# Optimization experiments

Hardware: AMD Instinct MI355X
Metric: run time of the kernel (lower is better)

The kernel has to match this reference:

```python
import jax, jax.numpy as jnp
import numpy as np

N, D_IN, D_HID, D_OUT, E = 8192, 1024, 4096, 1024, 8
N_ACTIVE = max(1, int(E * 0.625))  # 5
TEMP = float(np.e)               # temperature = np.e in source


def setup_inputs() -> dict:
    key = jax.random.key(0)
    ks = jax.random.split(key, 4)
    return {
        "x": jax.random.normal(ks[0], (N, D_IN), jnp.float32),
        "gate_w": jax.random.normal(ks[1], (D_IN, E), jnp.float32) * 0.02,
        "gate_b": jnp.zeros((E,), jnp.float32),
        "w1": jax.random.normal(ks[2], (E, D_IN, D_HID), jnp.float32) * 0.02,
        "b1": jnp.zeros((E, D_HID), jnp.float32),
        "w2": jax.random.normal(ks[3], (E, D_HID, D_OUT), jnp.float32) * 0.02,
        "b2": jnp.zeros((E, D_OUT), jnp.float32),
    }


def reference(x, gate_w, gate_b, w1, b1, w2, b2):
    # Gate: softmax over experts at temperature e, then top-k mask + renormalize
    scores = (x @ gate_w + gate_b) / TEMP                 # [N, E]
    probs = jax.nn.softmax(scores, axis=-1)               # [N, E]
    _, topk_idx = jax.lax.top_k(probs, N_ACTIVE)          # [N, k]
    mask = jax.nn.one_hot(topk_idx, E, dtype=probs.dtype).sum(axis=-2)  # [N, E]
    weights = probs * mask
    weights = weights / (weights.sum(axis=-1, keepdims=True) + 1e-8)
    # Dense all-experts FFN (dropout is eval-mode identity)
    h = jax.nn.relu(jnp.einsum('nd,edh->neh', x, w1) + b1)   # [N, E, d_hid]
    e_out = jnp.einsum('neh,eho->neo', h, w2) + b2           # [N, E, d_out]
    # Camp A (first E/2 experts) added, camp G subtracted: out = out_a - out_g
    sign = jnp.where(jnp.arange(E) < E // 2, 1.0, -1.0)      # [E]
    return jnp.einsum('ne,neo->no', weights * sign, e_out)   # [N, d_out]
```

## Files before the change

kernel.cpp:

```cpp
#include <hip/hip_runtime.h>
#include <hip/hip_bf16.h>
#include <cmath>


typedef _Float16 f16;
typedef _Float16 f16x8 __attribute__((ext_vector_type(8)));
typedef _Float16 f16x4 __attribute__((ext_vector_type(4)));
typedef float f32x4 __attribute__((ext_vector_type(4)));

#define NROWS 8192
#define DIN   1024
#define DHID  4096
#define DOUT  1024
#define NEXP  8

#define OFF_SGATE 0u
#define OFF_XH    262144u
#define OFF_W1T   17039360u
#define OFF_W2T   84148224u
#define OFF_P1    151257088u
#define OFF_HH    184811520u
#define NEED_NE2  319029248ull

__device__ __forceinline__ void gload_lds16(const void* gsrc, void* ldsdst) {
  __builtin_amdgcn_global_load_lds(
      (const __attribute__((address_space(1))) unsigned int*)gsrc,
      (__attribute__((address_space(3))) unsigned int*)ldsdst, 16, 0, 0);
}

__global__ void gate_kernel(const float* __restrict__ x,
                            const float* __restrict__ gw,
                            const float* __restrict__ gb,
                            float* __restrict__ sgate) {
  const int row = blockIdx.x * 4 + (threadIdx.x >> 6);
  const int l = threadIdx.x & 63;
  const float* xr = x + (size_t)row * DIN;
  float acc[8] = {0.f,0.f,0.f,0.f,0.f,0.f,0.f,0.f};
#pragma unroll
  for (int j = 0; j < 16; ++j) {
    const int k = l + 64 * j;
    const float xv = xr[k];
    const float4 g0 = *(const float4*)(gw + (size_t)k * 8);
    const float4 g1 = *(const float4*)(gw + (size_t)k * 8 + 4);
    acc[0] += xv * g0.x; acc[1] += xv * g0.y; acc[2] += xv * g0.z; acc[3] += xv * g0.w;
    acc[4] += xv * g1.x; acc[5] += xv * g1.y; acc[6] += xv * g1.z; acc[7] += xv * g1.w;
  }
#pragma unroll
  for (int off = 32; off > 0; off >>= 1) {
#pragma unroll
    for (int e = 0; e < 8; ++e) acc[e] += __shfl_xor(acc[e], off, 64);
  }
  if (l == 0) {
    const float invT = 0.36787944117144233f;
    float p[8]; float mx = -1e30f;
#pragma unroll
    for (int e = 0; e < 8; ++e) { p[e] = (acc[e] + gb[e]) * invT; mx = fmaxf(mx, p[e]); }
    float S = 0.f;
#pragma unroll
    for (int e = 0; e < 8; ++e) { p[e] = expf(p[e] - mx); S += p[e]; }
    const float inv = 1.0f / S;
#pragma unroll
    for (int e = 0; e < 8; ++e) p[e] *= inv;
    bool keep[8] = {true,true,true,true,true,true,true,true};
    for (int t = 0; t < 3; ++t) {
      float pmin = 1e30f; int mi = -1;
      for (int e = 0; e < 8; ++e)
        if (keep[e] && (p[e] < pmin || (p[e] == pmin && e > mi))) { pmin = p[e]; mi = e; }
      keep[mi] = false;
    }
    float wsum = 0.f;
#pragma unroll
    for (int e = 0; e < 8; ++e) if (keep[e]) wsum += p[e];
    const float rinv = 1.0f / (wsum + 1e-8f);
#pragma unroll
    for (int e = 0; e < 8; ++e) {
      const float wv = keep[e] ? p[e] * rinv : 0.0f;
      sgate[(size_t)row * 8 + e] = (e < 4) ? wv : -wv;
    }
  }
}

__global__ void cvt_x_kernel(const float* __restrict__ x, f16* __restrict__ xh) {
  const size_t i = ((size_t)blockIdx.x * blockDim.x + threadIdx.x) * 4;
  const float4 v = *(const float4*)(x + i);
  f16x4 o = { (f16)v.x, (f16)v.y, (f16)v.z, (f16)v.w };
  *(f16x4*)(xh + i) = o;
}

__global__ void transpose_cvt(const float* __restrict__ in, f16* __restrict__ out,
                              int R, int C) {
  __shared__ float tile[32][33];
  const int e = blockIdx.z;
  const float* ine = in + (size_t)e * R * C;
  f16* oute = out + (size_t)e * R * C;
  const int c0 = blockIdx.x * 32, r0 = blockIdx.y * 32;
  const int tx = threadIdx.x, ty = threadIdx.y;
#pragma unroll
  for (int i = 0; i < 4; ++i)
    tile[ty + i * 8][tx] = ine[(size_t)(r0 + ty + i * 8) * C + c0 + tx];
  __syncthreads();
#pragma unroll
  for (int i = 0; i < 4; ++i)
    oute[(size_t)(c0 + ty + i * 8) * R + r0 + tx] = (f16)tile[tx][ty + i * 8];
}

#define MFMAOP(a_, b_, c_) __builtin_amdgcn_mfma_f32_16x16x32_f16(a_, b_, c_, 0, 0, 0)

template <int EPI>
__global__ __launch_bounds__(512, 2) void gemm8p(
    const f16* __restrict__ A, int lda,
    const f16* __restrict__ B, int ldb, int nt,
    long long khA, long long khB,
    const float* __restrict__ bias,
    f16* __restrict__ outH, int ldc,
    float* outP0, float* outP1, int p1w,
    const float* __restrict__ sgate, int expert, int gx) {
  __shared__ alignas(16) f16 lA[4 * 8192];
  __shared__ alignas(16) f16 lB[4 * 8192];
  const int tid = threadIdx.x;
  const int l = tid & 63, w = tid >> 6;
  const int wr = w >> 2, wc = w & 3;

  const int nwg = gridDim.x, cpx = nwg >> 3;
  const int lg = ((int)blockIdx.x & 7) * cpx + ((int)blockIdx.x >> 3);

  int m0, n0;
  const f16* Aeff = A;
  const f16* Beff = B;
  float* P = nullptr;
  bool pw = false;
  if constexpr (EPI == 1) {
    m0 = (lg / gx) * 256; n0 = (lg % gx) * 256;
  } else {
    const int xx = lg >> 5, cc = lg & 31;
    const int kh = xx >> 2;
    n0 = (cc & 3) * 256;
    m0 = (((xx & 3) << 3) + (cc >> 2)) * 256;
    Aeff = A + (size_t)kh * (size_t)khA;
    Beff = B + (size_t)kh * (size_t)khB;
    P = kh ? outP1 : outP0;
    pw = (p1w != 0);
  }

  const int srow = tid >> 3;
  const int sxc = (tid & 7) ^ (srow & 7);
  const f16* pA = Aeff + (size_t)(m0 + srow) * lda + sxc * 8;
  const f16* pB = Beff + (size_t)(n0 + srow) * ldb + sxc * 8;
  f16* const dA = lA + w * 512;
  f16* const dB = lB + w * 512;

#define STG_A(slot, h, tk) do { \
    const f16* s_ = pA + (size_t)(h) * 128 * lda + (size_t)(tk) * 64; \
    gload_lds16(s_,            dA + (slot) * 8192); \
    gload_lds16(s_ + 64 * lda, dA + (slot) * 8192 + 4096); \
  } while (0)
#define STG_B(slot, h, tk) do { \
    const f16* s_ = pB + (size_t)(h) * 128 * ldb + (size_t)(tk) * 64; \
    gload_lds16(s_,            dB + (slot) * 8192); \
    gload_lds16(s_ + 64 * ldb, dB + (slot) * 8192 + 4096); \
  } while (0)

  const int cg = l >> 4, xr = l & 7;
  const int ok0 = ((cg ^ xr) << 4);
  const int ok1 = (((4 + cg) ^ xr) << 4);
  const char* const baA = (const char*)lA + (l & 15) * 128;
  const char* const baB = (const char*)lB + (wc & 1) * 8192 + (l & 15) * 128;

#define RDA(CA, f, o) (*(const f16x8*)(baA + ((CA) + wr) * 16384 + (f) * 2048 + (o)))
#define RDB(CB, g, o) (*(const f16x8*)(baB + ((CB) + (wc >> 1)) * 16384 + (g) * 2048 + (o)))
#define SYNC() do { __builtin_amdgcn_s_barrier(); \
    asm volatile("s_waitcnt lgkmcnt(0)" ::: "memory"); \
    __builtin_amdgcn_sched_barrier(0); } while (0)
#define ENDPH() do { __builtin_amdgcn_s_setprio(0); \
    __builtin_amdgcn_s_barrier(); } while (0)
#define VM6() do { asm volatile("s_waitcnt vmcnt(6)" ::: "memory"); \
    __builtin_amdgcn_sched_barrier(0); } while (0)
#define VM0() do { asm volatile("s_waitcnt vmcnt(0)" ::: "memory"); \
    __builtin_amdgcn_sched_barrier(0); } while (0)
#define MM(f, g, ar, br) acc[f][g] = MFMAOP(ar, br, acc[f][g])

  f32x4 acc[8][4] = {};
  f16x8 aA0,aA1,aB0,aB1,aC0,aC1,aD0,aD1;
  f16x8 b00,b01,b10,b11,b20,b21,b30,b31;

#define TILEBODY(T, CA, CB, SB1, SB0n, SA0n, SA1n) do { \
     \
    aA0 = RDA(CA, 0, ok0); aA1 = RDA(CA, 0, ok1); \
    aB0 = RDA(CA, 1, ok0); aB1 = RDA(CA, 1, ok1); \
    aC0 = RDA(CA, 2, ok0); aC1 = RDA(CA, 2, ok1); \
    aD0 = RDA(CA, 3, ok0); aD1 = RDA(CA, 3, ok1); \
    b00 = RDB(CB, 0, ok0); b01 = RDB(CB, 0, ok1); \
    b10 = RDB(CB, 1, ok0); b11 = RDB(CB, 1, ok1); \
    if ((T) + 1 < nt) STG_B(SB1, 1, (T) + 1); \
    SYNC(); \
    __builtin_amdgcn_s_setprio(1); \
    MM(0,0,aA0,b00); MM(0,1,aA0,b10); MM(1,0,aB0,b00); MM(1,1,aB0,b10); \
    MM(2,0,aC0,b00); MM(2,1,aC0,b10); MM(3,0,aD0,b00); MM(3,1,aD0,b10); \
    MM(0,0,aA1,b01); MM(0,1,aA1,b11); MM(1,0,aB1,b01); MM(1,1,aB1,b11); \
    MM(2,0,aC1,b01); MM(2,1,aC1,b11); MM(3,0,aD1,b01); MM(3,1,aD1,b11); \
    ENDPH(); \
     \
    b20 = RDB(CB, 2, ok0); b21 = RDB(CB, 2, ok1); \
    b30 = RDB(CB, 3, ok0); b31 = RDB(CB, 3, ok1); \
    SYNC(); \
    __builtin_amdgcn_s_setprio(1); \
    MM(0,2,aA0,b20); MM(0,3,aA0,b30); MM(1,2,aB0,b20); MM(1,3,aB0,b30); \
    MM(2,2,aC0,b20); MM(2,3,aC0,b30); MM(3,2,aD0,b20); MM(3,3,aD0,b30); \
    MM(0,2,aA1,b21); MM(0,3,aA1,b31); MM(1,2,aB1,b21); MM(1,3,aB1,b31); \
    MM(2,2,aC1,b21); MM(2,3,aC1,b31); MM(3,2,aD1,b21); MM(3,3,aD1,b31); \
    ENDPH(); \
     \
    aA0 = RDA(CA, 4, ok0); aA1 = RDA(CA, 4, ok1); \
    aB0 = RDA(CA, 5, ok0); aB1 = RDA(CA, 5, ok1); \
    aC0 = RDA(CA, 6, ok0); aC1 = RDA(CA, 6, ok1); \
    aD0 = RDA(CA, 7, ok0); aD1 = RDA(CA, 7, ok1); \
    if ((T) + 2 < nt) STG_B(SB0n, 0, (T) + 2); \
    SYNC(); \
    __builtin_amdgcn_s_setprio(1); \
    MM(4,0,aA0,b00); MM(4,1,aA0,b10); MM(5,0,aB0,b00); MM(5,1,aB0,b10); \
    MM(6,0,aC0,b00); MM(6,1,aC0,b10); MM(7,0,aD0,b00); MM(7,1,aD0,b10); \
    MM(4,0,aA1,b01); MM(4,1,aA1,b11); MM(5,0,aB1,b01); MM(5,1,aB1,b11); \
    MM(6,0,aC1,b01); MM(6,1,aC1,b11); MM(7,0,aD1,b01); MM(7,1,aD1,b11); \
    ENDPH(); \
     \
    if ((T) + 2 < nt) { STG_A(SA0n, 0, (T) + 2); STG_A(SA1n, 1, (T) + 2); \
                        VM6(); } \
    else { VM0(); } \
    SYNC(); \
    __builtin_amdgcn_s_setprio(1); \
    MM(4,2,aA0,b20); MM(4,3,aA0,b30); MM(5,2,aB0,b20); MM(5,3,aB0,b30); \
    MM(6,2,aC0,b20); MM(6,3,aC0,b30); MM(7,2,aD0,b20); MM(7,3,aD0,b30); \
    MM(4,2,aA1,b21); MM(4,3,aA1,b31); MM(5,2,aB1,b21); MM(5,3,aB1,b31); \
    MM(6,2,aC1,b21); MM(6,3,aC1,b31); MM(7,2,aD1,b21); MM(7,3,aD1,b31); \
    ENDPH(); \
  } while (0)

  STG_A(0, 0, 0); STG_B(0, 0, 0); STG_A(1, 1, 0); STG_B(1, 1, 0);
  STG_A(2, 0, 1); STG_B(2, 0, 1); STG_A(3, 1, 1);
  asm volatile("s_waitcnt vmcnt(6)" ::: "memory");
  __builtin_amdgcn_s_barrier();

  for (int t = 0; t < nt; t += 2) {
    TILEBODY(t,     0, 0, 3, 0, 0, 1);
    TILEBODY(t + 1, 2, 2, 1, 2, 2, 3);
  }
  asm volatile("s_waitcnt vmcnt(0)" ::: "memory");

  if constexpr (EPI == 1) {
#pragma unroll
    for (int mi = 0; mi < 8; ++mi)
#pragma unroll
      for (int r = 0; r < 4; ++r) {
        const int row = m0 + wr * 128 + mi * 16 + (l >> 4) * 4 + r;
        const float sg = sgate[(size_t)row * 8 + expert];
#pragma unroll
        for (int ni = 0; ni < 4; ++ni) {
          const int col = n0 + wc * 64 + ni * 16 + (l & 15);
          const float v = acc[mi][ni][r] + bias[col];
          outH[(size_t)row * ldc + col] = (f16)(fmaxf(v, 0.0f) * sg);
        }
      }
  } else {
    float* const scr = (w < 4) ? (float*)lA + w * 4096
                               : (float*)lB + (w - 4) * 4096;
    const int hl = l >> 4, ll = l & 15;
#pragma unroll
    for (int p = 0; p < 2; ++p) {
#pragma unroll
      for (int mi4 = 0; mi4 < 4; ++mi4)
#pragma unroll
        for (int r = 0; r < 4; ++r) {
          const int rowl = mi4 * 16 + hl * 4 + r;
#pragma unroll
          for (int ni = 0; ni < 4; ++ni)
            scr[rowl * 64 + ni * 16 + ll] = acc[p * 4 + mi4][ni][r];
        }
#pragma unroll
      for (int i = 0; i < 16; ++i) {
        const int rowl = hl + i * 4;
        f32x4 v = *(const f32x4*)(scr + rowl * 64 + ll * 4);
        const int row = m0 + wr * 128 + p * 64 + rowl;
        const int col = n0 + wc * 64 + ll * 4;
        f32x4* gp = (f32x4*)(P + (size_t)row * 1024 + col);
        if (!pw) {
          const f32x4 g = *gp;
          v[0] += g[0]; v[1] += g[1]; v[2] += g[2]; v[3] += g[3];
        }
        *gp = v;
      }
    }
  }
#undef STG_A
#undef STG_B
#undef RDA
#undef RDB
#undef SYNC
#undef ENDPH
#undef VM6
#undef VM0
#undef MM
#undef TILEBODY
}

template <bool WITHP>
__global__ void finalize_out(const float* p0,
                             const float* __restrict__ p1,
                             const float* __restrict__ sgate,
                             const float* __restrict__ b2,
                             float* out) {
  const int i = blockIdx.x * 256 + threadIdx.x;
  const int n = i >> 8, c4 = i & 255;
  float4 a = make_float4(0.f, 0.f, 0.f, 0.f);
  if constexpr (WITHP) {
    const float4 u = ((const float4*)p0)[i];
    const float4 v = ((const float4*)p1)[i];
    a.x = u.x + v.x; a.y = u.y + v.y; a.z = u.z + v.z; a.w = u.w + v.w;
  }
  const float* sg = sgate + (size_t)n * 8;
#pragma unroll
  for (int e = 0; e < 8; ++e) {
    const float s = sg[e];
    const float4 bv = ((const float4*)(b2 + (size_t)e * 1024))[c4];
    a.x += s * bv.x; a.y += s * bv.y; a.z += s * bv.z; a.w += s * bv.w;
  }
  ((float4*)out)[i] = a;
}

extern "C" void kernel_launch(void* const* d_in, const int* in_sizes, int n_in,
                              void* d_out, int out_size, void* d_ws, size_t ws_size,
                              hipStream_t stream) {
  const float* x  = (const float*)d_in[0];
  const float* gw = (const float*)d_in[1];
  const float* gb = (const float*)d_in[2];
  const float* w1 = (const float*)d_in[3];
  const float* b1 = (const float*)d_in[4];
  const float* w2 = (const float*)d_in[5];
  const float* b2 = (const float*)d_in[6];
  float* out = (float*)d_out;

  char* ws = (char*)d_ws;
  float* sgate = (float*)(ws + OFF_SGATE);
  f16* xh  = (f16*)(ws + OFF_XH);
  f16* w1t = (f16*)(ws + OFF_W1T);
  f16* w2t = (f16*)(ws + OFF_W2T);
  float* p1 = (float*)(ws + OFF_P1);
  f16* hh  = (f16*)(ws + OFF_HH);

  const int NE = (ws_size >= NEED_NE2) ? 2 : 1;
  const int ngrp = NEXP / NE;

  gate_kernel<<<NROWS / 4, 256, 0, stream>>>(x, gw, gb, sgate);
  cvt_x_kernel<<<(NROWS * DIN) / (256 * 4), 256, 0, stream>>>(x, xh);
  transpose_cvt<<<dim3(DHID / 32, DIN / 32, NEXP), dim3(32, 8), 0, stream>>>(w1, w1t, DIN, DHID);
  transpose_cvt<<<dim3(DOUT / 32, DHID / 32, NEXP), dim3(32, 8), 0, stream>>>(w2, w2t, DHID, DOUT);

  const long long khA = (long long)NE * 2048;
  const long long khB = (NE == 2) ? (long long)DOUT * DHID
                                  : 2048LL;
  const int nt2 = NE * 32;
  for (int g = 0; g < ngrp; ++g) {
    for (int ei = 0; ei < NE; ++ei) {
      const int e = g * NE + ei;
      gemm8p<1><<<512, 512, 0, stream>>>(
          xh, DIN, w1t + (size_t)e * DHID * DIN, DIN, DIN / 64,
          0, 0,
          b1 + (size_t)e * DHID, hh + (size_t)ei * DHID, NE * DHID,
          nullptr, nullptr, 0, sgate, e, DHID / 256);
    }
    gemm8p<2><<<256, 512, 0, stream>>>(
        hh, NE * DHID, w2t + (size_t)g * NE * DOUT * DHID, DHID, nt2,
        khA, khB,
        nullptr, nullptr, 0, out, p1, (g == 0) ? 1 : 0, nullptr, 0, 0);
  }
  finalize_out<true><<<(NROWS * DOUT) / (256 * 4), 256, 0, stream>>>(
      out, p1, sgate, b2, out);
}
```

Measured before the change: 1.358 ms.

## Replace second-stage 256x256 GEMM with 128x128 tile kernel using more workgroups

The down-projection GEMM, which accumulates into the fp32 partial outputs, moves from the shared 256x256-tile, 512-thread kernel to a dedicated 128x128-tile, 256-thread kernel with double-buffered K=32 steps and 1024 workgroups. The first-stage kernel is specialised to its original epilogue. The aim is better occupancy and CU load balance for the second GEMM, which previously launched only 256 workgroups. In exchange, per-tile data reuse is lower, global traffic is higher, and the simpler pipeline waits on vmcnt(0) every K step.

```diff
diff --git a/kernel.cpp b/kernel.cpp
--- a/kernel.cpp
+++ b/kernel.cpp
@@ -106,14 +106,11 @@
 
 #define MFMAOP(a_, b_, c_) __builtin_amdgcn_mfma_f32_16x16x32_f16(a_, b_, c_, 0, 0, 0)
 
-template <int EPI>
-__global__ __launch_bounds__(512, 2) void gemm8p(
+__global__ __launch_bounds__(512, 2) void gemm8p1(
     const f16* __restrict__ A, int lda,
     const f16* __restrict__ B, int ldb, int nt,
-    long long khA, long long khB,
     const float* __restrict__ bias,
     f16* __restrict__ outH, int ldc,
-    float* outP0, float* outP1, int p1w,
     const float* __restrict__ sgate, int expert, int gx) {
   __shared__ alignas(16) f16 lA[4 * 8192];
   __shared__ alignas(16) f16 lB[4 * 8192];
@@ -123,29 +120,12 @@
 
   const int nwg = gridDim.x, cpx = nwg >> 3;
   const int lg = ((int)blockIdx.x & 7) * cpx + ((int)blockIdx.x >> 3);
-
-  int m0, n0;
-  const f16* Aeff = A;
-  const f16* Beff = B;
-  float* P = nullptr;
-  bool pw = false;
-  if constexpr (EPI == 1) {
-    m0 = (lg / gx) * 256; n0 = (lg % gx) * 256;
-  } else {
-    const int xx = lg >> 5, cc = lg & 31;
-    const int kh = xx >> 2;
-    n0 = (cc & 3) * 256;
-    m0 = (((xx & 3) << 3) + (cc >> 2)) * 256;
-    Aeff = A + (size_t)kh * (size_t)khA;
-    Beff = B + (size_t)kh * (size_t)khB;
-    P = kh ? outP1 : outP0;
-    pw = (p1w != 0);
-  }
+  const int m0 = (lg / gx) * 256, n0 = (lg % gx) * 256;
 
   const int srow = tid >> 3;
   const int sxc = (tid & 7) ^ (srow & 7);
-  const f16* pA = Aeff + (size_t)(m0 + srow) * lda + sxc * 8;
-  const f16* pB = Beff + (size_t)(n0 + srow) * ldb + sxc * 8;
+  const f16* pA = A + (size_t)(m0 + srow) * lda + sxc * 8;
+  const f16* pB = B + (size_t)(n0 + srow) * ldb + sxc * 8;
   f16* const dA = lA + w * 512;
   f16* const dB = lB + w * 512;
 
@@ -184,7 +164,6 @@
   f16x8 b00,b01,b10,b11,b20,b21,b30,b31;
 
 #define TILEBODY(T, CA, CB, SB1, SB0n, SA0n, SA1n) do { \
-     \
     aA0 = RDA(CA, 0, ok0); aA1 = RDA(CA, 0, ok1); \
     aB0 = RDA(CA, 1, ok0); aB1 = RDA(CA, 1, ok1); \
     aC0 = RDA(CA, 2, ok0); aC1 = RDA(CA, 2, ok1); \
@@ -199,7 +178,6 @@
     MM(0,0,aA1,b01); MM(0,1,aA1,b11); MM(1,0,aB1,b01); MM(1,1,aB1,b11); \
     MM(2,0,aC1,b01); MM(2,1,aC1,b11); MM(3,0,aD1,b01); MM(3,1,aD1,b11); \
     ENDPH(); \
-     \
     b20 = RDB(CB, 2, ok0); b21 = RDB(CB, 2, ok1); \
     b30 = RDB(CB, 3, ok0); b31 = RDB(CB, 3, ok1); \
     SYNC(); \
@@ -209,7 +187,6 @@
     MM(0,2,aA1,b21); MM(0,3,aA1,b31); MM(1,2,aB1,b21); MM(1,3,aB1,b31); \
     MM(2,2,aC1,b21); MM(2,3,aC1,b31); MM(3,2,aD1,b21); MM(3,3,aD1,b31); \
     ENDPH(); \
-     \
     aA0 = RDA(CA, 4, ok0); aA1 = RDA(CA, 4, ok1); \
     aB0 = RDA(CA, 5, ok0); aB1 = RDA(CA, 5, ok1); \
     aC0 = RDA(CA, 6, ok0); aC1 = RDA(CA, 6, ok1); \
@@ -222,7 +199,6 @@
     MM(4,0,aA1,b01); MM(4,1,aA1,b11); MM(5,0,aB1,b01); MM(5,1,aB1,b11); \
     MM(6,0,aC1,b01); MM(6,1,aC1,b11); MM(7,0,aD1,b01); MM(7,1,aD1,b11); \
     ENDPH(); \
-     \
     if ((T) + 2 < nt) { STG_A(SA0n, 0, (T) + 2); STG_A(SA1n, 1, (T) + 2); \
                         VM6(); } \
     else { VM0(); } \
@@ -246,50 +222,19 @@
   }
   asm volatile("s_waitcnt vmcnt(0)" ::: "memory");
 
-  if constexpr (EPI == 1) {
-#pragma unroll
-    for (int mi = 0; mi < 8; ++mi)
-#pragma unroll
-      for (int r = 0; r < 4; ++r) {
-        const int row = m0 + wr * 128 + mi * 16 + (l >> 4) * 4 + r;
-        const float sg = sgate[(size_t)row * 8 + expert];
-#pragma unroll
-        for (int ni = 0; ni < 4; ++ni) {
-          const int col = n0 + wc * 64 + ni * 16 + (l & 15);
-          const float v = acc[mi][ni][r] + bias[col];
-          outH[(size_t)row * ldc + col] = (f16)(fmaxf(v, 0.0f) * sg);
-        }
-      }
-  } else {
-    float* const scr = (w < 4) ? (float*)lA + w * 4096
-                               : (float*)lB + (w - 4) * 4096;
-    const int hl = l >> 4, ll = l & 15;
-#pragma unroll
-    for (int p = 0; p < 2; ++p) {
-#pragma unroll
-      for (int mi4 = 0; mi4 < 4; ++mi4)
-#pragma unroll
-        for (int r = 0; r < 4; ++r) {
-          const int rowl = mi4 * 16 + hl * 4 + r;
-#pragma unroll
-          for (int ni = 0; ni < 4; ++ni)
-            scr[rowl * 64 + ni * 16 + ll] = acc[p * 4 + mi4][ni][r];
-        }
-#pragma unroll
-      for (int i = 0; i < 16; ++i) {
-        const int rowl = hl + i * 4;
-        f32x4 v = *(const f32x4*)(scr + rowl * 64 + ll * 4);
-        const int row = m0 + wr * 128 + p * 64 + rowl;
-        const int col = n0 + wc * 64 + ll * 4;
-        f32x4* gp = (f32x4*)(P + (size_t)row * 1024 + col);
-        if (!pw) {
-          const f32x4 g = *gp;
-          v[0] += g[0]; v[1] += g[1]; v[2] += g[2]; v[3] += g[3];
-        }
-        *gp = v;
+#pragma unroll
+  for (int mi = 0; mi < 8; ++mi)
+#pragma unroll
+    for (int r = 0; r < 4; ++r) {
+      const int row = m0 + wr * 128 + mi * 16 + (l >> 4) * 4 + r;
+      const float sg = sgate[(size_t)row * 8 + expert];
+#pragma unroll
+      for (int ni = 0; ni < 4; ++ni) {
+        const int col = n0 + wc * 64 + ni * 16 + (l & 15);
+        const float v = acc[mi][ni][r] + bias[col];
+        outH[(size_t)row * ldc + col] = (f16)(fmaxf(v, 0.0f) * sg);
       }
     }
-  }
 #undef STG_A
 #undef STG_B
 #undef RDA
@@ -300,6 +245,119 @@
 #undef VM0
 #undef MM
 #undef TILEBODY
+}
+
+__global__ __launch_bounds__(256, 4) void gemm128_acc(
+    const f16* __restrict__ A, int lda,
+    const f16* __restrict__ B, int ldb, int nt,
+    long long khA, long long khB,
+    float* outP0, float* outP1, int p1w) {
+  __shared__ alignas(16) f16 lA[2 * 4096];
+  __shared__ alignas(16) f16 lB[2 * 4096];
+  const int tid = threadIdx.x;
+  const int l = tid & 63, w = tid >> 6;
+  const int wr = w >> 1, wc = w & 1;
+
+  const int nwg = gridDim.x, cpx = nwg >> 3;
+  const int lg = ((int)blockIdx.x & 7) * cpx + ((int)blockIdx.x >> 3);
+  const int xx = lg >> 7, cc = lg & 127;
+  const int kh = xx >> 2;
+  const int m0 = (((xx & 3) << 4) + (cc >> 3)) * 128;
+  const int n0 = (cc & 7) * 128;
+  const f16* Aeff = A + (size_t)kh * (size_t)khA;
+  const f16* Beff = B + (size_t)kh * (size_t)khB;
+  float* P = kh ? outP1 : outP0;
+  const bool pw = (p1w != 0);
+
+  const int srow = tid >> 2;
+  const int ssw = (srow & 3) ^ ((srow >> 2) & 3);
+  const int sxc = (tid & 3) ^ ssw;
+  const f16* pA = Aeff + (size_t)(m0 + srow) * lda + sxc * 8;
+  const f16* pB = Beff + (size_t)(n0 + srow) * ldb + sxc * 8;
+
+#define STG_A(buf, tk) do { \
+    const f16* s_ = pA + (size_t)(tk) * 32; \
+    gload_lds16(s_,            lA + (buf) * 4096 + w * 512); \
+    gload_lds16(s_ + 64 * lda, lA + (buf) * 4096 + 2048 + w * 512); \
+  } while (0)
+#define STG_B(buf, tk) do { \
+    const f16* s_ = pB + (size_t)(tk) * 32; \
+    gload_lds16(s_,            lB + (buf) * 4096 + w * 512); \
+    gload_lds16(s_ + 64 * ldb, lB + (buf) * 4096 + 2048 + w * 512); \
+  } while (0)
+
+  const int cg = l >> 4;
+  int aoff[4], boff[4];
+#pragma unroll
+  for (int f = 0; f < 4; ++f) {
+    const int ra = wr * 64 + f * 16 + (l & 15);
+    aoff[f] = ra * 64 + ((cg ^ ((ra & 3) ^ ((ra >> 2) & 3))) << 4);
+    const int rb = wc * 64 + f * 16 + (l & 15);
+    boff[f] = rb * 64 + ((cg ^ ((rb & 3) ^ ((rb >> 2) & 3))) << 4);
+  }
+#define RA(buf, f) (*(const f16x8*)((const char*)lA + (buf) * 8192 + aoff[f]))
+#define RB(buf, g) (*(const f16x8*)((const char*)lB + (buf) * 8192 + boff[g]))
+#define MM(f, g, ar, br) acc[f][g] = MFMAOP(ar, br, acc[f][g])
+
+  f32x4 acc[4][4] = {};
+  f16x8 a0, a1, a2, a3, b0, b1, b2, b3;
+
+#define KSTEP(T, BUF, NBUF) do { \
+    if ((T) + 1 < nt) { STG_A(NBUF, (T) + 1); STG_B(NBUF, (T) + 1); } \
+    a0 = RA(BUF, 0); a1 = RA(BUF, 1); a2 = RA(BUF, 2); a3 = RA(BUF, 3); \
+    b0 = RB(BUF, 0); b1 = RB(BUF, 1); b2 = RB(BUF, 2); b3 = RB(BUF, 3); \
+    __builtin_amdgcn_s_setprio(1); \
+    MM(0,0,a0,b0); MM(0,1,a0,b1); MM(0,2,a0,b2); MM(0,3,a0,b3); \
+    MM(1,0,a1,b0); MM(1,1,a1,b1); MM(1,2,a1,b2); MM(1,3,a1,b3); \
+    MM(2,0,a2,b0); MM(2,1,a2,b1); MM(2,2,a2,b2); MM(2,3,a2,b3); \
+    MM(3,0,a3,b0); MM(3,1,a3,b1); MM(3,2,a3,b2); MM(3,3,a3,b3); \
+    __builtin_amdgcn_s_setprio(0); \
+    asm volatile("s_waitcnt vmcnt(0)" ::: "memory"); \
+    __builtin_amdgcn_s_barrier(); \
+  } while (0)
+
+  STG_A(0, 0); STG_B(0, 0);
+  asm volatile("s_waitcnt vmcnt(0)" ::: "memory");
+  __builtin_amdgcn_s_barrier();
+
+  for (int t = 0; t < nt; t += 2) {
+    KSTEP(t,     0, 1);
+    KSTEP(t + 1, 1, 0);
+  }
+
+  float* const scr = (float*)lA + w * 2048;
+  const int hl = l >> 4, ll = l & 15;
+#pragma unroll
+  for (int p = 0; p < 2; ++p) {
+#pragma unroll
+    for (int mi2 = 0; mi2 < 2; ++mi2)
+#pragma unroll
+      for (int r = 0; r < 4; ++r) {
+        const int rowl = mi2 * 16 + hl * 4 + r;
+#pragma unroll
+        for (int ni = 0; ni < 4; ++ni)
+          scr[rowl * 64 + ni * 16 + ll] = acc[p * 2 + mi2][ni][r];
+      }
+#pragma unroll
+    for (int i = 0; i < 8; ++i) {
+      const int rowl = hl + i * 4;
+      f32x4 v = *(const f32x4*)(scr + rowl * 64 + ll * 4);
+      const int row = m0 + wr * 64 + p * 32 + rowl;
+      const int col = n0 + wc * 64 + ll * 4;
+      f32x4* gp = (f32x4*)(P + (size_t)row * 1024 + col);
+      if (!pw) {
+        const f32x4 g = *gp;
+        v[0] += g[0]; v[1] += g[1]; v[2] += g[2]; v[3] += g[3];
+      }
+      *gp = v;
+    }
+  }
+#undef STG_A
+#undef STG_B
+#undef RA
+#undef RB
+#undef MM
+#undef KSTEP
 }
 
 template <bool WITHP>
@@ -357,20 +415,18 @@
   const long long khA = (long long)NE * 2048;
   const long long khB = (NE == 2) ? (long long)DOUT * DHID
                                   : 2048LL;
-  const int nt2 = NE * 32;
+  const int nt2 = NE * 2048 / 32;
   for (int g = 0; g < ngrp; ++g) {
     for (int ei = 0; ei < NE; ++ei) {
       const int e = g * NE + ei;
-      gemm8p<1><<<512, 512, 0, stream>>>(
+      gemm8p1<<<512, 512, 0, stream>>>(
           xh, DIN, w1t + (size_t)e * DHID * DIN, DIN, DIN / 64,
-          0, 0,
           b1 + (size_t)e * DHID, hh + (size_t)ei * DHID, NE * DHID,
-          nullptr, nullptr, 0, sgate, e, DHID / 256);
+          sgate, e, DHID / 256);
     }
-    gemm8p<2><<<256, 512, 0, stream>>>(
+    gemm128_acc<<<1024, 256, 0, stream>>>(
         hh, NE * DHID, w2t + (size_t)g * NE * DOUT * DHID, DHID, nt2,
-        khA, khB,
-        nullptr, nullptr, 0, out, p1, (g == 0) ? 1 : 0, nullptr, 0, 0);
+        khA, khB, out, p1, (g == 0) ? 1 : 0);
   }
   finalize_out<true><<<(NROWS * DOUT) / (256 * 4), 256, 0, stream>>>(
       out, p1, sgate, b2, out);
```

New measurement: 1.419 ms. 1.05x slower.
